# Performance work log

Hardware: AMD Instinct MI355X
Metric: run time of the kernel (lower is better)

The kernel has to match this reference:

```python
import jax, jax.numpy as jnp
import numpy as np

SHIFT = 1  # shift_direction fixed to +1 (module draws +/-1 at random)


def setup_inputs() -> dict:
    key = jax.random.key(0)
    k1, k2 = jax.random.split(key)
    x = jax.random.normal(k1, (128, 48, 28, 28), dtype=jnp.float32)
    w = jax.random.normal(k2, (24, 96, 7), dtype=jnp.float32)  # (Cin, Cout, K) per group, shared across groups
    return {"x": x, "w": w}


def reference(x, w):
    B, H, W = 128, 28, 28
    G, CIN, COUT, K = 2, 24, 96, 7
    # x -> (B, G, Cin, H, W); the unfold/einsum is a grouped conv1d over W (axis 'm'),
    # with H (axis 'n') untouched -> fold H into the batch dim.
    x5 = x.reshape(B, G, CIN, H, W)
    xc = x5.transpose(0, 3, 1, 2, 4).reshape(B * H, G * CIN, W)  # (B*H, 48, W)
    # kernel (Cout, Cin, K); same weights for both groups -> tile to (G*Cout, Cin, K)
    kern = jnp.tile(jnp.transpose(w, (1, 0, 2)), (G, 1, 1))  # (192, 24, 7)
    y = jax.lax.conv_general_dilated(
        xc, kern, window_strides=(1,), padding=[(3, 3)],
        dimension_numbers=('NCH', 'OIH', 'NCH'), feature_group_count=G)  # (B*H, 192, W)
    y = y.reshape(B, H, G * COUT, W).transpose(0, 2, 1, 3)  # (B, 192, H, W), channels group-major = (o, i)
    return jnp.roll(y, SHIFT, axis=2)  # roll along H (original dim 2)
```

## Files before the change

kernel.cpp:

```cpp
#include <hip/hip_runtime.h>


typedef __attribute__((ext_vector_type(8))) short short8;
typedef __attribute__((ext_vector_type(4))) float float4v;

#define B_     128
#define H_     28
#define W_     28
#define CIN_   24
#define COUT_  96
#define K_     7
#define KSTEPS 6
#define NT_    6
#define YSLD   114

static __device__ __forceinline__ unsigned f2bf_u(float f) {
    union { float f; unsigned u; } v; v.f = f;
    return (v.u + 0x7fffu + ((v.u >> 16) & 1u)) >> 16;
}
static __device__ __forceinline__ short f2bf(float f) { return (short)f2bf_u(f); }

__global__ __launch_bounds__(64)
void wfrag_kernel(const float* __restrict__ w, short8* __restrict__ wf) {
    const int idx  = blockIdx.x;
    const int ks   = idx / 6, nt = idx - ks * 6;
    const int lane = threadIdx.x;
    const int c    = nt * 16 + (lane & 15);
    const int q    = ks * 4 + (lane >> 4);
    short8 v;
    if (q < 21) {
        const int k   = (q * 11) >> 5;
        const int ci0 = (q - 3 * k) * 8;
#pragma unroll
        for (int j = 0; j < 8; ++j)
            v[j] = f2bf(w[(ci0 + j) * (COUT_ * K_) + c * K_ + k]);
    } else {
#pragma unroll
        for (int j = 0; j < 8; ++j) v[j] = 0;
    }
    wf[idx * 64 + lane] = v;
}

__global__ __launch_bounds__(448)
void conv_mfma_kernel(const float* __restrict__ x,
                      const float4* __restrict__ wfg,
                      float* __restrict__ out) {
    const int bid = blockIdx.x;
    const int g   = bid & 1;
    const int hq  = (bid >> 1) % 7;
    const int b   = bid / 14;
    const int h0  = hq * 4;
    const int tid = threadIdx.x;

    __shared__ __align__(16) char smem[6912 + 36864];
    short*  xs  = (short*)smem;
    short8* wfl = (short8*)(smem + 6912);
    float*  ys0 = (float*)(smem + 6912);
    float*  ys1 = (float*)(smem + 6912 + 16 * YSLD * 4);

    {
        float4* wdst = (float4*)(smem + 6912);
        for (int i = tid; i < 2304; i += 448) wdst[i] = wfg[i];
    }

    for (int idx = tid; idx < 4 * 12 * 36; idx += 448) {
        const int p  = idx % 36;
        const int t2 = idx / 36;
        const int cp = t2 % 12;
        const int hl = t2 / 12;
        const int ws = p - 3;
        float v0 = 0.0f, v1 = 0.0f;
        if (ws >= 0 && ws < W_) {
            const size_t base = ((size_t)(b * 48 + g * CIN_ + cp * 2) * H_ + (h0 + hl)) * W_ + ws;
            v0 = x[base];
            v1 = x[base + (size_t)H_ * W_];
        }
        ((unsigned*)xs)[(hl * 36 + p) * 12 + cp] = f2bf_u(v0) | (f2bf_u(v1) << 16);
    }
    __syncthreads();

    const int lane = tid & 63;
    const int wv   = tid >> 6;
    const int cgrp = lane & 15;
    const int kgrp = lane >> 4;

    const int mA = wv * 16 + cgrp;
    const int hA = mA / 28;
    const int tA = mA - hA * 28;

    int sidx[KSTEPS];
#pragma unroll
    for (int ks = 0; ks < KSTEPS; ++ks) {
        const int q   = ks * 4 + kgrp;
        const int k   = (q * 11) >> 5;
        const int ci0 = (q - 3 * k) * 8;
        sidx[ks] = (hA * 36 + tA + k) * 24 + ci0;
    }

    float4v acc[NT_];
#pragma unroll
    for (int i = 0; i < NT_; ++i) acc[i] = (float4v)(0.0f);

#pragma unroll
    for (int ks = 0; ks < KSTEPS; ++ks) {
        const short8 a = *(const short8*)&xs[sidx[ks]];
        short8 br[NT_];
#pragma unroll
        for (int nt = 0; nt < NT_; ++nt)
            br[nt] = wfl[(ks * NT_ + nt) * 64 + lane];
#pragma unroll
        for (int nt = 0; nt < NT_; ++nt)
            acc[nt] = __builtin_amdgcn_mfma_f32_16x16x32_bf16(a, br[nt], acc[nt], 0, 0, 0);
    }

    __syncthreads();

    const int m0 = wv * 16 + kgrp * 4;
    const int cS   = tid / 28;
    const int remS = tid % 28;
    const int hlS  = remS / 7;
    const int fS   = remS % 7;
    int hd = h0 + hlS + 1; if (hd >= H_) hd -= H_;

#pragma unroll
    for (int nt = 0; nt < NT_; ++nt) {
        if (nt) __syncthreads();
        float* ys = (nt & 1) ? ys1 : ys0;
        *(float2*)&ys[cgrp * YSLD + m0]     = make_float2(acc[nt][0], acc[nt][1]);
        *(float2*)&ys[cgrp * YSLD + m0 + 2] = make_float2(acc[nt][2], acc[nt][3]);
        __syncthreads();
        const float2 u0 = *(const float2*)&ys[cS * YSLD + hlS * 28 + 4 * fS];
        const float2 u1 = *(const float2*)&ys[cS * YSLD + hlS * 28 + 4 * fS + 2];
        float4 v; v.x = u0.x; v.y = u0.y; v.z = u1.x; v.w = u1.y;
        *(float4*)&out[(((size_t)b * 192 + g * COUT_ + nt * 16 + cS) * H_ + hd) * W_ + 4 * fS] = v;
    }
}

extern "C" void kernel_launch(void* const* d_in, const int* in_sizes, int n_in,
                              void* d_out, int out_size, void* d_ws, size_t ws_size,
                              hipStream_t stream) {
    const float* x = (const float*)d_in[0];
    const float* w = (const float*)d_in[1];
    float* out = (float*)d_out;
    short8* wf = (short8*)d_ws;

    wfrag_kernel<<<36, 64, 0, stream>>>(w, wf);
    conv_mfma_kernel<<<B_ * 7 * 2, 448, 0, stream>>>(x, (const float4*)wf, out);
}
```

Measured before the change: 34.16 us.

## Read weights from global, store outputs directly, drop LDS staging

Weight fragments are now read straight from global memory (L2/L1 cached) instead of being copied into shared memory, and the LDS transpose used for output staging is removed. Each lane writes its accumulator values directly as scalar stores. The LDS footprint shrinks to the input tile only and several barriers go away, with a launch bound hint of 6 blocks per CU to raise occupancy. In exchange, output stores become scalar and less coalesced (16 channels by 4 positions per wave), and weight loads go through global memory on every block.

```diff
diff --git a/kernel.cpp b/kernel.cpp
--- a/kernel.cpp
+++ b/kernel.cpp
@@ -12,7 +12,6 @@
 #define K_     7
 #define KSTEPS 6
 #define NT_    6
-#define YSLD   114
 
 static __device__ __forceinline__ unsigned f2bf_u(float f) {
     union { float f; unsigned u; } v; v.f = f;
@@ -41,9 +40,9 @@
     wf[idx * 64 + lane] = v;
 }
 
-__global__ __launch_bounds__(448)
+__global__ __launch_bounds__(448, 6)
 void conv_mfma_kernel(const float* __restrict__ x,
-                      const float4* __restrict__ wfg,
+                      const short8* __restrict__ wfg,
                       float* __restrict__ out) {
     const int bid = blockIdx.x;
     const int g   = bid & 1;
@@ -52,16 +51,7 @@
     const int h0  = hq * 4;
     const int tid = threadIdx.x;
 
-    __shared__ __align__(16) char smem[6912 + 36864];
-    short*  xs  = (short*)smem;
-    short8* wfl = (short8*)(smem + 6912);
-    float*  ys0 = (float*)(smem + 6912);
-    float*  ys1 = (float*)(smem + 6912 + 16 * YSLD * 4);
-
-    {
-        float4* wdst = (float4*)(smem + 6912);
-        for (int i = tid; i < 2304; i += 448) wdst[i] = wfg[i];
-    }
+    __shared__ __align__(16) short xs[4 * 36 * 24];
 
     for (int idx = tid; idx < 4 * 12 * 36; idx += 448) {
         const int p  = idx % 36;
@@ -107,32 +97,27 @@
         short8 br[NT_];
 #pragma unroll
         for (int nt = 0; nt < NT_; ++nt)
-            br[nt] = wfl[(ks * NT_ + nt) * 64 + lane];
+            br[nt] = wfg[(ks * NT_ + nt) * 64 + lane];
 #pragma unroll
         for (int nt = 0; nt < NT_; ++nt)
             acc[nt] = __builtin_amdgcn_mfma_f32_16x16x32_bf16(a, br[nt], acc[nt], 0, 0, 0);
     }
 
-    __syncthreads();
-
-    const int m0 = wv * 16 + kgrp * 4;
-    const int cS   = tid / 28;
-    const int remS = tid % 28;
-    const int hlS  = remS / 7;
-    const int fS   = remS % 7;
-    int hd = h0 + hlS + 1; if (hd >= H_) hd -= H_;
-
+    int offj[4];
+#pragma unroll
+    for (int j = 0; j < 4; ++j) {
+        const int m  = wv * 16 + kgrp * 4 + j;
+        const int hl = m / 28;
+        const int t  = m - hl * 28;
+        int hd = h0 + hl + 1; if (hd >= H_) hd -= H_;
+        offj[j] = hd * W_ + t;
+    }
+    float* cbase = out + ((size_t)(b * 192 + g * COUT_ + cgrp)) * (H_ * W_);
 #pragma unroll
     for (int nt = 0; nt < NT_; ++nt) {
-        if (nt) __syncthreads();
-        float* ys = (nt & 1) ? ys1 : ys0;
-        *(float2*)&ys[cgrp * YSLD + m0]     = make_float2(acc[nt][0], acc[nt][1]);
-        *(float2*)&ys[cgrp * YSLD + m0 + 2] = make_float2(acc[nt][2], acc[nt][3]);
-        __syncthreads();
-        const float2 u0 = *(const float2*)&ys[cS * YSLD + hlS * 28 + 4 * fS];
-        const float2 u1 = *(const float2*)&ys[cS * YSLD + hlS * 28 + 4 * fS + 2];
-        float4 v; v.x = u0.x; v.y = u0.y; v.z = u1.x; v.w = u1.y;
-        *(float4*)&out[(((size_t)b * 192 + g * COUT_ + nt * 16 + cS) * H_ + hd) * W_ + 4 * fS] = v;
+#pragma unroll
+        for (int j = 0; j < 4; ++j)
+            cbase[nt * 16 * (H_ * W_) + offj[j]] = acc[nt][j];
     }
 }
 
@@ -145,5 +130,5 @@
     short8* wf = (short8*)d_ws;
 
     wfrag_kernel<<<36, 64, 0, stream>>>(w, wf);
-    conv_mfma_kernel<<<B_ * 7 * 2, 448, 0, stream>>>(x, (const float4*)wf, out);
+    conv_mfma_kernel<<<B_ * 7 * 2, 448, 0, stream>>>(x, wf, out);
 }
```

Measured after the change: 39.89 us. 16.8% more time.
